# Optimization experiments

Hardware: AMD Instinct MI355X
Metric: run time of the kernel (lower is better)

## Reference

```python
import jax, jax.numpy as jnp
import numpy as np

NFEAT, NHID, NCLASS = 256, 128, 40
N_NODES, N_EDGES = 50000, 800000
BN_EPS = 1e-5


def setup_inputs() -> dict:
    key = jax.random.key(0)
    ks = jax.random.split(key, 8)
    x = jax.random.normal(ks[0], (N_NODES, NFEAT), dtype=jnp.float32)
    edge_index = jax.random.randint(ks[1], (2, N_EDGES), 0, N_NODES, dtype=jnp.int64)
    # GCNConv layer 0: nfeat -> nhid (Glorot-ish scale)
    W0 = jax.random.normal(ks[2], (NFEAT, NHID), dtype=jnp.float32) / np.sqrt(NFEAT)
    b0 = jnp.zeros((NHID,), dtype=jnp.float32)
    # BatchNorm1d(nhid)
    gamma0 = jnp.ones((NHID,), dtype=jnp.float32)
    beta0 = jnp.zeros((NHID,), dtype=jnp.float32)
    # GCNConv last: nhid -> nclass
    W1 = jax.random.normal(ks[3], (NHID, NCLASS), dtype=jnp.float32) / np.sqrt(NHID)
    b1 = jnp.zeros((NCLASS,), dtype=jnp.float32)
    return {"x": x, "edge_index": edge_index, "W0": W0, "b0": b0,
            "gamma0": gamma0, "beta0": beta0, "W1": W1, "b1": b1}


def _gcn_conv(x, src, dst, W, b, num_nodes):
    # normalize=False GCNConv: linear transform then raw sum aggregation src->dst
    h = x @ W                                   # [N, out]
    out = jax.ops.segment_sum(h[src], dst, num_segments=num_nodes)
    return out + b


def reference(x, edge_index, W0, b0, gamma0, beta0, W1, b1):
    N = x.shape[0]
    src, dst = edge_index[0], edge_index[1]
    # layer 0 conv
    h = _gcn_conv(x, src, dst, W0, b0, N)       # [N, nhid]
    # BatchNorm1d (training-mode batch stats, biased variance)
    mu = h.mean(axis=0)
    var = jnp.mean((h - mu) ** 2, axis=0)
    h = gamma0 * (h - mu) * jax.lax.rsqrt(var + BN_EPS) + beta0
    h = jax.nn.relu(h)
    # (dropout skipped: deterministic eval baseline)
    # last conv (early-return path in original forward)
    out = _gcn_conv(h, src, dst, W1, b1, N)     # [N, nclass]
    return out
```

## Files before the change

kernel.cpp:

```cpp
#include <hip/hip_runtime.h>
#include <hip/hip_fp8.h>

#define NFEAT 256
#define NHID 128
#define NCLASS 40
#define NNODES 50000
#define NEDGES 800000
#define BN_EPS 1e-5f
#define NBK 196
#define NBLK 100
#define EPB 8000
#define BKCAP 6144
#define NW1 6250
#define GEMM1_BLOCKS 1563

typedef __attribute__((ext_vector_type(4))) float f32x4;
typedef __attribute__((ext_vector_type(8))) short bf16x8;

__device__ inline ushort f2bf(float f) {
    uint u = __float_as_uint(f);
    u += 0x7FFF + ((u >> 16) & 1);
    return (ushort)(u >> 16);
}
__device__ inline float bflo(uint v) { return __uint_as_float(v << 16); }
__device__ inline float bfhi(uint v) { return __uint_as_float(v & 0xFFFF0000u); }

__device__ inline uint pk_fp8x4(float a0, float a1, float a2, float a3) {
#if __has_builtin(__builtin_amdgcn_cvt_pk_fp8_f32)
    int u = 0;
    u = __builtin_amdgcn_cvt_pk_fp8_f32(a0, a1, u, false);
    u = __builtin_amdgcn_cvt_pk_fp8_f32(a2, a3, u, true);
    return (uint)u;
#else
    __hip_fp8_e4m3 q0(a0), q1(a1), q2(a2), q3(a3);
    return (uint)q0.__x | ((uint)q1.__x << 8) | ((uint)q2.__x << 16) | ((uint)q3.__x << 24);
#endif
}
__device__ inline float fp8lo(uint v) {
#if __has_builtin(__builtin_amdgcn_cvt_f32_fp8)
    return __builtin_amdgcn_cvt_f32_fp8((int)v, 0);
#else
    __hip_fp8_e4m3 q; q.__x = (__hip_fp8_storage_t)(v & 0xFF); return (float)q;
#endif
}
__device__ inline float fp8hi(uint v) {
#if __has_builtin(__builtin_amdgcn_cvt_f32_fp8)
    return __builtin_amdgcn_cvt_f32_fp8((int)v, 1);
#else
    __hip_fp8_e4m3 q; q.__x = (__hip_fp8_storage_t)((v >> 8) & 0xFF); return (float)q;
#endif
}

__global__ void k_prep(const float* __restrict__ W0, ushort* __restrict__ W0F,
                       const int* __restrict__ ei, int* __restrict__ bcnt) {
    __shared__ int cnt[NBK];
    if (blockIdx.x < 16) {
        const int t = blockIdx.x * 256 + threadIdx.x;
        const int lane = t & 63;
        const int grp = t >> 6;
        const int kc = grp & 7, fi = grp >> 3;
        const int n = fi * 16 + (lane & 15);
        const int k0 = kc * 32 + (lane >> 4) * 8;
        ushort v[8];
        #pragma unroll
        for (int j = 0; j < 8; ++j) v[j] = f2bf(W0[(k0 + j) * NHID + n]);
        uint4 u;
        u.x = (uint)v[0] | ((uint)v[1] << 16);
        u.y = (uint)v[2] | ((uint)v[3] << 16);
        u.z = (uint)v[4] | ((uint)v[5] << 16);
        u.w = (uint)v[6] | ((uint)v[7] << 16);
        *(uint4*)&W0F[(grp * 64 + lane) * 8] = u;
    } else {
        const int blk = blockIdx.x - 16;
        const int t = threadIdx.x;
        if (t < NBK) cnt[t] = 0;
        __syncthreads();
        const int base = blk * EPB;
        for (int i = t; i < EPB; i += 256)
            atomicAdd(&cnt[ei[NEDGES + base + i] >> 8], 1);
        __syncthreads();
        if (t < NBK) bcnt[blk * NBK + t] = cnt[t];
    }
}

__global__ void k_bkscan(const int* __restrict__ bcnt, int* __restrict__ off,
                         int* __restrict__ bstart, int* __restrict__ rowptr,
                         float* __restrict__ stats) {
    __shared__ int sc[256];
    const int t = threadIdx.x;
    stats[t] = 0.f;
    int tot = 0;
    if (t < NBK)
        for (int b = 0; b < NBLK; ++b) tot += bcnt[b * NBK + t];
    sc[t] = tot;
    __syncthreads();
    for (int o = 1; o < 256; o <<= 1) {
        const int v = (t >= o) ? sc[t - o] : 0;
        __syncthreads();
        sc[t] += v;
        __syncthreads();
    }
    const int excl = sc[t] - tot;
    if (t < NBK) bstart[t] = excl;
    else if (t == NBK) bstart[NBK] = sc[NBK - 1];
    if (t == 0) rowptr[NNODES] = NEDGES;
    if (t < NBK) {
        int run = excl;
        for (int b = 0; b < NBLK; ++b) { off[b * NBK + t] = run; run += bcnt[b * NBK + t]; }
    }
}

__launch_bounds__(256, 1)
__global__ void k_scatter_gemm1(const int* __restrict__ ei, const int* __restrict__ off,
                                uint* __restrict__ packed,
                                const float* __restrict__ x, const ushort* __restrict__ W0F,
                                uchar* __restrict__ h1) {
    __shared__ int cur[NBK];
    if (blockIdx.x < NBLK) {
        const int t = threadIdx.x, blk = blockIdx.x;
        if (t < NBK) cur[t] = off[blk * NBK + t];
        __syncthreads();
        const int base = blk * EPB;
        for (int i = t; i < EPB; i += 256) {
            const int src = ei[base + i];
            const int dst = ei[NEDGES + base + i];
            const int pos = atomicAdd(&cur[dst >> 8], 1);
            packed[pos] = (uint)src | ((uint)(dst & 255) << 16);
        }
    } else {
        const int gt = (blockIdx.x - NBLK) * 256 + threadIdx.x;
        const int w = gt >> 6;
        if (w >= NW1) return;
        const int lane = gt & 63;
        const int half = w & 1;
        const int node = (w >> 1) * 16 + (lane & 15);
        const int nclamp = node < NNODES ? node : NNODES - 1;
        const float* xg = &x[(long)nclamp * NFEAT + (lane >> 4) * 8];

        float4 xa[8], xb[8];
        #pragma unroll
        for (int kc = 0; kc < 8; ++kc) {
            xa[kc] = *(const float4*)(xg + kc * 32);
            xb[kc] = *(const float4*)(xg + kc * 32 + 4);
        }
        __builtin_amdgcn_sched_barrier(0);
        bf16x8 xf[8];
        #pragma unroll
        for (int kc = 0; kc < 8; ++kc) {
            xf[kc][0]=(short)f2bf(xa[kc].x); xf[kc][1]=(short)f2bf(xa[kc].y);
            xf[kc][2]=(short)f2bf(xa[kc].z); xf[kc][3]=(short)f2bf(xa[kc].w);
            xf[kc][4]=(short)f2bf(xb[kc].x); xf[kc][5]=(short)f2bf(xb[kc].y);
            xf[kc][6]=(short)f2bf(xb[kc].z); xf[kc][7]=(short)f2bf(xb[kc].w);
        }
        __builtin_amdgcn_sched_barrier(0);
        f32x4 acc[4];
        #pragma unroll
        for (int f = 0; f < 4; ++f) acc[f] = (f32x4){0.f, 0.f, 0.f, 0.f};
        const ushort* wbase = &W0F[(size_t)lane * 8];
        #pragma unroll
        for (int kc = 0; kc < 8; ++kc) {
            #pragma unroll
            for (int f = 0; f < 4; ++f) {
                const int grp = (half * 4 + f) * 8 + kc;
                const bf16x8 wf = *(const bf16x8*)&wbase[(size_t)grp * 64 * 8];
                acc[f] = __builtin_amdgcn_mfma_f32_16x16x32_bf16(wf, xf[kc], acc[f], 0, 0, 0);
            }
        }
        if (node < NNODES) {
            const int nq = (lane >> 4) * 4;
            uchar* hp = &h1[(long)node * NHID + half * 64 + nq];
            #pragma unroll
            for (int f = 0; f < 4; ++f)
                *(uint*)&hp[f * 16] = pk_fp8x4(acc[f][0], acc[f][1], acc[f][2], acc[f][3]);
        }
    }
}

__launch_bounds__(256)
__global__ void k_bksort(const uint* __restrict__ packed, const int* __restrict__ bstart,
                         int* __restrict__ esrc, int* __restrict__ rowptr) {
    __shared__ uint pr[BKCAP];
    __shared__ int cnt[256], sc[256], cur[256];
    const int t = threadIdx.x, b = blockIdx.x;
    const int nb = bstart[b], ne = bstart[b + 1];
    const int n = ne - nb;
    cnt[t] = 0;
    __syncthreads();
    for (int i = t; i < n; i += 256) {
        const uint p = packed[nb + i];
        pr[i] = p;
        atomicAdd(&cnt[p >> 16], 1);
    }
    __syncthreads();
    const int v = cnt[t];
    sc[t] = v;
    __syncthreads();
    for (int o = 1; o < 256; o <<= 1) {
        const int tmp = (t >= o) ? sc[t - o] : 0;
        __syncthreads();
        sc[t] += tmp;
        __syncthreads();
    }
    const int excl = sc[t] - v;
    cur[t] = excl;
    const int node = (b << 8) + t;
    if (node < NNODES) rowptr[node] = nb + excl;
    __syncthreads();
    for (int i = t; i < n; i += 256) {
        const uint p = pr[i];
        const int pos = atomicAdd(&cur[p >> 16], 1);
        esrc[nb + pos] = (int)(p & 0xFFFFu);
    }
}

__launch_bounds__(256)
__global__ void k_gather1(const int* __restrict__ rowptr, const int* __restrict__ esrc,
                          const uchar* __restrict__ h1, const float* __restrict__ b0,
                          float* __restrict__ agg1) {
    const int w = (blockIdx.x * blockDim.x + threadIdx.x) >> 6;
    const int lane = threadIdx.x & 63;
    if (w >= NNODES) return;
    const int beg = rowptr[w], end = rowptr[w + 1];
    const int f = lane * 2;
    float2 acc = *(const float2*)&b0[f];
    int i = beg;
    for (; i + 7 < end; i += 8) {
        uint v[8];
        #pragma unroll
        for (int j = 0; j < 8; ++j)
            v[j] = (uint)*(const ushort*)&h1[(long)esrc[i + j] * NHID + f];
        #pragma unroll
        for (int j = 0; j < 8; ++j) { acc.x += fp8lo(v[j]); acc.y += fp8hi(v[j]); }
    }
    for (; i < end; ++i) {
        const uint v = (uint)*(const ushort*)&h1[(long)esrc[i] * NHID + f];
        acc.x += fp8lo(v); acc.y += fp8hi(v);
    }
    *(float2*)&agg1[(long)w * NHID + f] = acc;
}

__global__ void k_bnstats(const float* __restrict__ agg1,
                          float* __restrict__ sums, float* __restrict__ sumsq) {
    __shared__ float sd[256 * 4], sd2[256 * 4];
    const int t = threadIdx.x;
    const int c4 = (t & 31) * 4;
    const int rr = t >> 5;
    float4 s = make_float4(0.f,0.f,0.f,0.f), s2 = s;
    for (int r = blockIdx.x * 8 + rr; r < NNODES; r += gridDim.x * 8) {
        const float4 v = *(const float4*)&agg1[(long)r * NHID + c4];
        s.x += v.x; s.y += v.y; s.z += v.z; s.w += v.w;
        s2.x += v.x*v.x; s2.y += v.y*v.y; s2.z += v.z*v.z; s2.w += v.w*v.w;
    }
    *(float4*)&sd[t * 4] = s; *(float4*)&sd2[t * 4] = s2;
    __syncthreads();
    if (t < 32) {
        #pragma unroll
        for (int j = 1; j < 8; ++j) {
            const float4 a = *(const float4*)&sd[(j * 32 + t) * 4];
            const float4 a2 = *(const float4*)&sd2[(j * 32 + t) * 4];
            s = *(float4*)&sd[t * 4];
            s2 = *(float4*)&sd2[t * 4];
            s.x += a.x; s.y += a.y; s.z += a.z; s.w += a.w;
            s2.x += a2.x; s2.y += a2.y; s2.z += a2.z; s2.w += a2.w;
            *(float4*)&sd[t * 4] = s; *(float4*)&sd2[t * 4] = s2;
        }
        atomicAdd(&sums[c4 + 0], s.x);  atomicAdd(&sums[c4 + 1], s.y);
        atomicAdd(&sums[c4 + 2], s.z);  atomicAdd(&sums[c4 + 3], s.w);
        atomicAdd(&sumsq[c4 + 0], s2.x); atomicAdd(&sumsq[c4 + 1], s2.y);
        atomicAdd(&sumsq[c4 + 2], s2.z); atomicAdd(&sumsq[c4 + 3], s2.w);
    }
}

__launch_bounds__(256)
__global__ void k_gemm2(const float* __restrict__ agg1, const float* __restrict__ W1,
                        const float* __restrict__ sums, const float* __restrict__ sumsq,
                        const float* __restrict__ gamma, const float* __restrict__ beta,
                        ushort* __restrict__ h2) {
    __shared__ float xs[64 * 132];
    __shared__ float wt[40 * 132];
    __shared__ float s_scale[128], s_shift[128];
    const int t = threadIdx.x;
    const int base = blockIdx.x * 64;

    if (t < NHID) {
        const float mu = sums[t] * (1.f / NNODES);
        float var = sumsq[t] * (1.f / NNODES) - mu * mu;
        var = fmaxf(var, 0.f);
        const float sc = gamma[t] * rsqrtf(var + BN_EPS);
        s_scale[t] = sc;
        s_shift[t] = beta[t] - mu * sc;
    }
    for (int idx = t; idx < NHID * NCLASS; idx += 256) {
        const int c = idx / NCLASS, j = idx % NCLASS;
        wt[j * 132 + c] = W1[idx];
    }
    __syncthreads();
    {
        const int cc = (t & 31) * 4;
        const float4 sc = *(const float4*)&s_scale[cc];
        const float4 sh = *(const float4*)&s_shift[cc];
        const int rb = t >> 5;
        #pragma unroll
        for (int p = 0; p < 8; ++p) {
            const int row = p * 8 + rb;
            const int g = base + row;
            float4 v = make_float4(0.f, 0.f, 0.f, 0.f);
            if (g < NNODES) {
                const float4 a = *(const float4*)&agg1[(long)g * NHID + cc];
                v.x = fmaxf(a.x * sc.x + sh.x, 0.f);
                v.y = fmaxf(a.y * sc.y + sh.y, 0.f);
                v.z = fmaxf(a.z * sc.z + sh.z, 0.f);
                v.w = fmaxf(a.w * sc.w + sh.w, 0.f);
            }
            *(float4*)&xs[row * 132 + cc] = v;
        }
    }
    __syncthreads();

    const int node = t >> 2;
    const int j0 = (t & 3) * 10;
    float acc[10] = {};
    for (int c4 = 0; c4 < 32; ++c4) {
        const int c = c4 * 4;
        const float4 a = *(const float4*)&xs[node * 132 + c];
        #pragma unroll
        for (int jj = 0; jj < 10; ++jj) {
            const float4 wv = *(const float4*)&wt[(j0 + jj) * 132 + c];
            acc[jj] += a.x * wv.x + a.y * wv.y + a.z * wv.z + a.w * wv.w;
        }
    }
    const int g = base + node;
    if (g < NNODES) {
        #pragma unroll
        for (int p = 0; p < 5; ++p) {
            uint u = (uint)f2bf(acc[2 * p]) | ((uint)f2bf(acc[2 * p + 1]) << 16);
            *(uint*)&h2[(long)g * NCLASS + j0 + 2 * p] = u;
        }
    }
}

__launch_bounds__(256)
__global__ void k_gather2(const int* __restrict__ rowptr, const int* __restrict__ esrc,
                          const ushort* __restrict__ h2, const float* __restrict__ b1,
                          float* __restrict__ out) {
    const int t = threadIdx.x;
    if (t >= 240) return;
    const int node = blockIdx.x * 12 + t / 20;
    if (node >= NNODES) return;
    const int f = (t % 20) * 2;
    const int beg = rowptr[node], end = rowptr[node + 1];
    float2 acc = make_float2(b1[f], b1[f + 1]);
    int i = beg;
    for (; i + 3 < end; i += 4) {
        const uint v0 = *(const uint*)&h2[(long)esrc[i]     * NCLASS + f];
        const uint v1 = *(const uint*)&h2[(long)esrc[i + 1] * NCLASS + f];
        const uint v2 = *(const uint*)&h2[(long)esrc[i + 2] * NCLASS + f];
        const uint v3 = *(const uint*)&h2[(long)esrc[i + 3] * NCLASS + f];
        acc.x += (bflo(v0) + bflo(v1)) + (bflo(v2) + bflo(v3));
        acc.y += (bfhi(v0) + bfhi(v1)) + (bfhi(v2) + bfhi(v3));
    }
    for (; i < end; ++i) {
        const uint v = *(const uint*)&h2[(long)esrc[i] * NCLASS + f];
        acc.x += bflo(v); acc.y += bfhi(v);
    }
    *(float2*)&out[(long)node * NCLASS + f] = acc;
}

extern "C" void kernel_launch(void* const* d_in, const int* in_sizes, int n_in,
                              void* d_out, int out_size, void* d_ws, size_t ws_size,
                              hipStream_t stream) {
    const float* x      = (const float*)d_in[0];
    const int*   ei     = (const int*)d_in[1];
    const float* W0     = (const float*)d_in[2];
    const float* b0     = (const float*)d_in[3];
    const float* gamma0 = (const float*)d_in[4];
    const float* beta0  = (const float*)d_in[5];
    const float* W1     = (const float*)d_in[6];
    const float* b1     = (const float*)d_in[7];
    float* out = (float*)d_out;

    char* ws = (char*)d_ws;
    float* sums  = (float*)ws;
    float* sumsq = sums + 128;
    int* wsI     = (int*)(ws + 4096);
    int* rowptr  = wsI;
    int* esrc    = wsI + 50048;
    int* bcnt    = wsI + 850048;
    int* off     = wsI + 869696;
    int* bstart  = wsI + 889344;
    ushort* W0F  = (ushort*)(ws + 3563520);
    uchar* h1    = (uchar*)(ws + 3629056);
    float* agg1  = (float*)(ws + 16429056);
    uint* packed = (uint*)agg1;
    ushort* h2   = (ushort*)h1;

    k_prep<<<16 + NBLK, 256, 0, stream>>>(W0, W0F, ei, bcnt);
    k_bkscan<<<1, 256, 0, stream>>>(bcnt, off, bstart, rowptr, sums);
    k_scatter_gemm1<<<NBLK + GEMM1_BLOCKS, 256, 0, stream>>>(ei, off, packed, x, W0F, h1);
    k_bksort<<<NBK, 256, 0, stream>>>(packed, bstart, esrc, rowptr);
    k_gather1<<<(NNODES * 64 + 255) / 256, 256, 0, stream>>>(rowptr, esrc, h1, b0, agg1);
    k_bnstats<<<256, 256, 0, stream>>>(agg1, sums, sumsq);
    k_gemm2<<<(NNODES + 63) / 64, 256, 0, stream>>>(agg1, W1, sums, sumsq, gamma0, beta0, h2);
    k_gather2<<<(NNODES + 11) / 12, 256, 0, stream>>>(rowptr, esrc, h2, b1, out);
}
```

Measured before the change: 169.2 us.

## Pre-convert x to bf16 in prep kernel and stage GEMM1 tiles through swizzled LDS

Adds an fp32-to-bf16 conversion pass for x to the k_prep kernel, writing a bf16 copy of x into workspace. The GEMM1 blocks now load 64 rows of bf16 x into LDS with an XOR swizzle, using global_load_lds when the builtin is available. Each wave then computes all 128 output features for its 16 rows instead of half of them, so x is read once per row rather than twice. The aim is to take the in-kernel conversion off the GEMM path and remove the duplicated x loads. The cost is an extra round trip of the bf16 copy through memory (one write, one read), so total traffic may not shrink.

```diff
diff --git a/kernel.cpp b/kernel.cpp
--- a/kernel.cpp
+++ b/kernel.cpp
@@ -11,8 +11,8 @@
 #define NBLK 100
 #define EPB 8000
 #define BKCAP 6144
-#define NW1 6250
-#define GEMM1_BLOCKS 1563
+#define XCVT_BLOCKS 1563
+#define GEMM1_BLOCKS 782
 
 typedef __attribute__((ext_vector_type(4))) float f32x4;
 typedef __attribute__((ext_vector_type(8))) short bf16x8;
@@ -52,7 +52,8 @@
 }
 
 __global__ void k_prep(const float* __restrict__ W0, ushort* __restrict__ W0F,
-                       const int* __restrict__ ei, int* __restrict__ bcnt) {
+                       const int* __restrict__ ei, int* __restrict__ bcnt,
+                       const float* __restrict__ x, ushort* __restrict__ xbf) {
     __shared__ int cnt[NBK];
     if (blockIdx.x < 16) {
         const int t = blockIdx.x * 256 + threadIdx.x;
@@ -70,7 +71,7 @@
         u.z = (uint)v[4] | ((uint)v[5] << 16);
         u.w = (uint)v[6] | ((uint)v[7] << 16);
         *(uint4*)&W0F[(grp * 64 + lane) * 8] = u;
-    } else {
+    } else if (blockIdx.x < 16 + NBLK) {
         const int blk = blockIdx.x - 16;
         const int t = threadIdx.x;
         if (t < NBK) cnt[t] = 0;
@@ -80,6 +81,18 @@
             atomicAdd(&cnt[ei[NEDGES + base + i] >> 8], 1);
         __syncthreads();
         if (t < NBK) bcnt[blk * NBK + t] = cnt[t];
+    } else {
+        const float4* x4 = (const float4*)x;
+        const int tid = (blockIdx.x - 16 - NBLK) * 256 + threadIdx.x;
+        for (int i = tid; i < NNODES * NFEAT / 8; i += XCVT_BLOCKS * 256) {
+            const float4 a = x4[2 * i], b = x4[2 * i + 1];
+            uint4 u;
+            u.x = (uint)f2bf(a.x) | ((uint)f2bf(a.y) << 16);
+            u.y = (uint)f2bf(a.z) | ((uint)f2bf(a.w) << 16);
+            u.z = (uint)f2bf(b.x) | ((uint)f2bf(b.y) << 16);
+            u.w = (uint)f2bf(b.z) | ((uint)f2bf(b.w) << 16);
+            *(uint4*)&xbf[(size_t)i * 8] = u;
+        }
     }
 }
 
@@ -113,10 +126,11 @@
 __launch_bounds__(256, 1)
 __global__ void k_scatter_gemm1(const int* __restrict__ ei, const int* __restrict__ off,
                                 uint* __restrict__ packed,
-                                const float* __restrict__ x, const ushort* __restrict__ W0F,
+                                const ushort* __restrict__ xbf, const ushort* __restrict__ W0F,
                                 uchar* __restrict__ h1) {
-    __shared__ int cur[NBK];
+    __shared__ __align__(16) uchar lds[32768];
     if (blockIdx.x < NBLK) {
+        int* cur = (int*)lds;
         const int t = threadIdx.x, blk = blockIdx.x;
         if (t < NBK) cur[t] = off[blk * NBK + t];
         __syncthreads();
@@ -128,50 +142,54 @@
             packed[pos] = (uint)src | ((uint)(dst & 255) << 16);
         }
     } else {
-        const int gt = (blockIdx.x - NBLK) * 256 + threadIdx.x;
-        const int w = gt >> 6;
-        if (w >= NW1) return;
-        const int lane = gt & 63;
-        const int half = w & 1;
-        const int node = (w >> 1) * 16 + (lane & 15);
-        const int nclamp = node < NNODES ? node : NNODES - 1;
-        const float* xg = &x[(long)nclamp * NFEAT + (lane >> 4) * 8];
-
-        float4 xa[8], xb[8];
+        const int t = threadIdx.x;
+        const int lane = t & 63;
+        const int wave = t >> 6;
+        const int block_row = (blockIdx.x - NBLK) * 64;
+
+        #pragma unroll
+        for (int i = 0; i < 8; ++i) {
+            const int ig = wave * 8 + i;
+            const int B = (ig * 64 + lane) * 16;
+            const int row = B >> 9;
+            const int chunk = (B >> 4) & 31;
+            const int srow = min(block_row + row, NNODES - 1);
+            const ushort* gsrc = &xbf[(size_t)srow * NFEAT + (size_t)((chunk ^ (row & 7)) * 8)];
+#if __has_builtin(__builtin_amdgcn_global_load_lds)
+            __builtin_amdgcn_global_load_lds(
+                (const __attribute__((address_space(1))) void*)gsrc,
+                (__attribute__((address_space(3))) void*)(lds + ig * 1024), 16, 0, 0);
+#else
+            *(uint4*)(lds + ig * 1024 + lane * 16) = *(const uint4*)gsrc;
+#endif
+        }
+        __syncthreads();
+
+        const int r = wave * 16 + (lane & 15);
+        const int cbase = lane >> 4;
+        f32x4 acc[8];
+        #pragma unroll
+        for (int f = 0; f < 8; ++f) acc[f] = (f32x4){0.f, 0.f, 0.f, 0.f};
+        const ushort* wbase = &W0F[(size_t)lane * 8];
+
         #pragma unroll
         for (int kc = 0; kc < 8; ++kc) {
-            xa[kc] = *(const float4*)(xg + kc * 32);
-            xb[kc] = *(const float4*)(xg + kc * 32 + 4);
-        }
-        __builtin_amdgcn_sched_barrier(0);
-        bf16x8 xf[8];
-        #pragma unroll
-        for (int kc = 0; kc < 8; ++kc) {
-            xf[kc][0]=(short)f2bf(xa[kc].x); xf[kc][1]=(short)f2bf(xa[kc].y);
-            xf[kc][2]=(short)f2bf(xa[kc].z); xf[kc][3]=(short)f2bf(xa[kc].w);
-            xf[kc][4]=(short)f2bf(xb[kc].x); xf[kc][5]=(short)f2bf(xb[kc].y);
-            xf[kc][6]=(short)f2bf(xb[kc].z); xf[kc][7]=(short)f2bf(xb[kc].w);
-        }
-        __builtin_amdgcn_sched_barrier(0);
-        f32x4 acc[4];
-        #pragma unroll
-        for (int f = 0; f < 4; ++f) acc[f] = (f32x4){0.f, 0.f, 0.f, 0.f};
-        const ushort* wbase = &W0F[(size_t)lane * 8];
-        #pragma unroll
-        for (int kc = 0; kc < 8; ++kc) {
+            const int chunk = (kc * 4 + cbase) ^ (r & 7);
+            const bf16x8 xf = *(const bf16x8*)(lds + r * 512 + chunk * 16);
             #pragma unroll
-            for (int f = 0; f < 4; ++f) {
-                const int grp = (half * 4 + f) * 8 + kc;
-                const bf16x8 wf = *(const bf16x8*)&wbase[(size_t)grp * 64 * 8];
-                acc[f] = __builtin_amdgcn_mfma_f32_16x16x32_bf16(wf, xf[kc], acc[f], 0, 0, 0);
+            for (int fi = 0; fi < 8; ++fi) {
+                const bf16x8 wf = *(const bf16x8*)&wbase[(size_t)(fi * 8 + kc) * 64 * 8];
+                acc[fi] = __builtin_amdgcn_mfma_f32_16x16x32_bf16(wf, xf, acc[fi], 0, 0, 0);
             }
         }
+
+        const int node = block_row + r;
         if (node < NNODES) {
             const int nq = (lane >> 4) * 4;
-            uchar* hp = &h1[(long)node * NHID + half * 64 + nq];
+            uchar* hp = &h1[(long)node * NHID + nq];
             #pragma unroll
-            for (int f = 0; f < 4; ++f)
-                *(uint*)&hp[f * 16] = pk_fp8x4(acc[f][0], acc[f][1], acc[f][2], acc[f][3]);
+            for (int fi = 0; fi < 8; ++fi)
+                *(uint*)&hp[fi * 16] = pk_fp8x4(acc[fi][0], acc[fi][1], acc[fi][2], acc[fi][3]);
         }
     }
 }
@@ -392,11 +410,12 @@
     uchar* h1    = (uchar*)(ws + 3629056);
     float* agg1  = (float*)(ws + 16429056);
     uint* packed = (uint*)agg1;
+    ushort* xbf  = (ushort*)(ws + 20623360);
     ushort* h2   = (ushort*)h1;
 
-    k_prep<<<16 + NBLK, 256, 0, stream>>>(W0, W0F, ei, bcnt);
+    k_prep<<<16 + NBLK + XCVT_BLOCKS, 256, 0, stream>>>(W0, W0F, ei, bcnt, x, xbf);
     k_bkscan<<<1, 256, 0, stream>>>(bcnt, off, bstart, rowptr, sums);
-    k_scatter_gemm1<<<NBLK + GEMM1_BLOCKS, 256, 0, stream>>>(ei, off, packed, x, W0F, h1);
+    k_scatter_gemm1<<<NBLK + GEMM1_BLOCKS, 256, 0, stream>>>(ei, off, packed, xbf, W0F, h1);
     k_bksort<<<NBK, 256, 0, stream>>>(packed, bstart, esrc, rowptr);
     k_gather1<<<(NNODES * 64 + 255) / 256, 256, 0, stream>>>(rowptr, esrc, h1, b0, agg1);
     k_bnstats<<<256, 256, 0, stream>>>(agg1, sums, sumsq);
```

New measurement: 174.0 us. 2.9% more time.

## Merge prep, scan, scatter, bucket sort and GEMM1 into one persistent kernel

Applied to the files above, without the earlier changes.

Four launches (W0 repack plus edge counting, bucket scan, scatter plus GEMM1, bucket sort) become one kernel. Block roles are split by block index and ordered with global atomic flags and spin-waits, and a memset clears the flags and stats. The aim is to cut launch gaps and let GEMM1 overlap the edge sort. The cost is that the spin-waits rely on the producer blocks being scheduled before the consumers, so deadlock is possible if they are not, and the bucket sort now reads packed from global memory twice and recomputes the scan in every block.

```diff
diff --git a/kernel.cpp b/kernel.cpp
--- a/kernel.cpp
+++ b/kernel.cpp
@@ -10,7 +10,6 @@
 #define NBK 196
 #define NBLK 100
 #define EPB 8000
-#define BKCAP 6144
 #define NW1 6250
 #define GEMM1_BLOCKS 1563
 
@@ -51,13 +50,29 @@
 #endif
 }
 
-__global__ void k_prep(const float* __restrict__ W0, ushort* __restrict__ W0F,
-                       const int* __restrict__ ei, int* __restrict__ bcnt) {
-    __shared__ int cnt[NBK];
-    if (blockIdx.x < 16) {
-        const int t = blockIdx.x * 256 + threadIdx.x;
-        const int lane = t & 63;
-        const int grp = t >> 6;
+__device__ inline void spin_eq(int* f, int target) {
+    while (__hip_atomic_load(f, __ATOMIC_ACQUIRE, __HIP_MEMORY_SCOPE_AGENT) != target)
+        __builtin_amdgcn_s_sleep(8);
+}
+__device__ inline void release_inc(int* f) {
+    __hip_atomic_fetch_add(f, 1, __ATOMIC_RELEASE, __HIP_MEMORY_SCOPE_AGENT);
+}
+
+__launch_bounds__(256)
+__global__ void k_mega(const float* __restrict__ W0, ushort* __restrict__ W0F,
+                       const int* __restrict__ ei, int* __restrict__ bcnt,
+                       uint* __restrict__ packed, int* __restrict__ esrc,
+                       int* __restrict__ rowptr,
+                       const float* __restrict__ x, uchar* __restrict__ h1,
+                       int* __restrict__ flags) {
+    __shared__ int s_cnt[256], s_sc[256], s_cur[256];
+    __shared__ int s_seg[2];
+    int* f0 = flags; int* f1 = flags + 1; int* f2 = flags + 2;
+    const int bid = blockIdx.x, tid = threadIdx.x;
+
+    if (bid < 16) {
+        const int t = bid * 256 + tid;
+        const int lane = t & 63, grp = t >> 6;
         const int kc = grp & 7, fi = grp >> 3;
         const int n = fi * 16 + (lane & 15);
         const int k0 = kc * 32 + (lane >> 4) * 8;
@@ -70,146 +85,147 @@
         u.z = (uint)v[4] | ((uint)v[5] << 16);
         u.w = (uint)v[6] | ((uint)v[7] << 16);
         *(uint4*)&W0F[(grp * 64 + lane) * 8] = u;
-    } else {
-        const int blk = blockIdx.x - 16;
-        const int t = threadIdx.x;
-        if (t < NBK) cnt[t] = 0;
-        __syncthreads();
+        if (bid == 0 && tid == 0) rowptr[NNODES] = NEDGES;
+        __threadfence();
+        __syncthreads();
+        if (tid == 0) release_inc(f0);
+        return;
+    }
+
+    if (bid < 16 + NBLK) {
+        const int blk = bid - 16;
         const int base = blk * EPB;
-        for (int i = t; i < EPB; i += 256)
-            atomicAdd(&cnt[ei[NEDGES + base + i] >> 8], 1);
-        __syncthreads();
-        if (t < NBK) bcnt[blk * NBK + t] = cnt[t];
-    }
-}
-
-__global__ void k_bkscan(const int* __restrict__ bcnt, int* __restrict__ off,
-                         int* __restrict__ bstart, int* __restrict__ rowptr,
-                         float* __restrict__ stats) {
-    __shared__ int sc[256];
-    const int t = threadIdx.x;
-    stats[t] = 0.f;
-    int tot = 0;
-    if (t < NBK)
-        for (int b = 0; b < NBLK; ++b) tot += bcnt[b * NBK + t];
-    sc[t] = tot;
-    __syncthreads();
-    for (int o = 1; o < 256; o <<= 1) {
-        const int v = (t >= o) ? sc[t - o] : 0;
-        __syncthreads();
-        sc[t] += v;
-        __syncthreads();
-    }
-    const int excl = sc[t] - tot;
-    if (t < NBK) bstart[t] = excl;
-    else if (t == NBK) bstart[NBK] = sc[NBK - 1];
-    if (t == 0) rowptr[NNODES] = NEDGES;
-    if (t < NBK) {
-        int run = excl;
-        for (int b = 0; b < NBLK; ++b) { off[b * NBK + t] = run; run += bcnt[b * NBK + t]; }
-    }
-}
-
-__launch_bounds__(256, 1)
-__global__ void k_scatter_gemm1(const int* __restrict__ ei, const int* __restrict__ off,
-                                uint* __restrict__ packed,
-                                const float* __restrict__ x, const ushort* __restrict__ W0F,
-                                uchar* __restrict__ h1) {
-    __shared__ int cur[NBK];
-    if (blockIdx.x < NBLK) {
-        const int t = threadIdx.x, blk = blockIdx.x;
-        if (t < NBK) cur[t] = off[blk * NBK + t];
-        __syncthreads();
-        const int base = blk * EPB;
-        for (int i = t; i < EPB; i += 256) {
+        if (tid < NBK) s_cnt[tid] = 0;
+        __syncthreads();
+        for (int i = tid; i < EPB; i += 256)
+            atomicAdd(&s_cnt[ei[NEDGES + base + i] >> 8], 1);
+        __syncthreads();
+        if (tid < NBK) bcnt[blk * NBK + tid] = s_cnt[tid];
+        __threadfence();
+        __syncthreads();
+        if (tid == 0) { release_inc(f1); spin_eq(f1, NBLK); }
+        __syncthreads();
+        int tot = 0, pre = 0;
+        if (tid < NBK) {
+            for (int bb = 0; bb < NBLK; ++bb) {
+                const int v = bcnt[bb * NBK + tid];
+                tot += v;
+                if (bb < blk) pre += v;
+            }
+        }
+        s_sc[tid] = tot;
+        __syncthreads();
+        for (int o = 1; o < 256; o <<= 1) {
+            const int v = (tid >= o) ? s_sc[tid - o] : 0;
+            __syncthreads();
+            s_sc[tid] += v;
+            __syncthreads();
+        }
+        s_cur[tid] = (s_sc[tid] - tot) + pre;
+        __syncthreads();
+        for (int i = tid; i < EPB; i += 256) {
             const int src = ei[base + i];
             const int dst = ei[NEDGES + base + i];
-            const int pos = atomicAdd(&cur[dst >> 8], 1);
+            const int pos = atomicAdd(&s_cur[dst >> 8], 1);
             packed[pos] = (uint)src | ((uint)(dst & 255) << 16);
         }
-    } else {
-        const int gt = (blockIdx.x - NBLK) * 256 + threadIdx.x;
-        const int w = gt >> 6;
-        if (w >= NW1) return;
-        const int lane = gt & 63;
-        const int half = w & 1;
-        const int node = (w >> 1) * 16 + (lane & 15);
-        const int nclamp = node < NNODES ? node : NNODES - 1;
-        const float* xg = &x[(long)nclamp * NFEAT + (lane >> 4) * 8];
-
-        float4 xa[8], xb[8];
-        #pragma unroll
-        for (int kc = 0; kc < 8; ++kc) {
-            xa[kc] = *(const float4*)(xg + kc * 32);
-            xb[kc] = *(const float4*)(xg + kc * 32 + 4);
-        }
-        __builtin_amdgcn_sched_barrier(0);
-        bf16x8 xf[8];
-        #pragma unroll
-        for (int kc = 0; kc < 8; ++kc) {
-            xf[kc][0]=(short)f2bf(xa[kc].x); xf[kc][1]=(short)f2bf(xa[kc].y);
-            xf[kc][2]=(short)f2bf(xa[kc].z); xf[kc][3]=(short)f2bf(xa[kc].w);
-            xf[kc][4]=(short)f2bf(xb[kc].x); xf[kc][5]=(short)f2bf(xb[kc].y);
-            xf[kc][6]=(short)f2bf(xb[kc].z); xf[kc][7]=(short)f2bf(xb[kc].w);
-        }
-        __builtin_amdgcn_sched_barrier(0);
-        f32x4 acc[4];
-        #pragma unroll
-        for (int f = 0; f < 4; ++f) acc[f] = (f32x4){0.f, 0.f, 0.f, 0.f};
-        const ushort* wbase = &W0F[(size_t)lane * 8];
-        #pragma unroll
-        for (int kc = 0; kc < 8; ++kc) {
-            #pragma unroll
-            for (int f = 0; f < 4; ++f) {
-                const int grp = (half * 4 + f) * 8 + kc;
-                const bf16x8 wf = *(const bf16x8*)&wbase[(size_t)grp * 64 * 8];
-                acc[f] = __builtin_amdgcn_mfma_f32_16x16x32_bf16(wf, xf[kc], acc[f], 0, 0, 0);
-            }
-        }
-        if (node < NNODES) {
-            const int nq = (lane >> 4) * 4;
-            uchar* hp = &h1[(long)node * NHID + half * 64 + nq];
-            #pragma unroll
-            for (int f = 0; f < 4; ++f)
-                *(uint*)&hp[f * 16] = pk_fp8x4(acc[f][0], acc[f][1], acc[f][2], acc[f][3]);
-        }
-    }
-}
-
-__launch_bounds__(256)
-__global__ void k_bksort(const uint* __restrict__ packed, const int* __restrict__ bstart,
-                         int* __restrict__ esrc, int* __restrict__ rowptr) {
-    __shared__ uint pr[BKCAP];
-    __shared__ int cnt[256], sc[256], cur[256];
-    const int t = threadIdx.x, b = blockIdx.x;
-    const int nb = bstart[b], ne = bstart[b + 1];
-    const int n = ne - nb;
-    cnt[t] = 0;
+        __threadfence();
+        __syncthreads();
+        if (tid == 0) release_inc(f2);
+        return;
+    }
+
+    if (bid < 16 + NBLK + NBK) {
+        const int b = bid - 16 - NBLK;
+        if (tid == 0) spin_eq(f2, NBLK);
+        __syncthreads();
+        int tot = 0;
+        if (tid < NBK)
+            for (int bb = 0; bb < NBLK; ++bb) tot += bcnt[bb * NBK + tid];
+        s_sc[tid] = tot;
+        __syncthreads();
+        for (int o = 1; o < 256; o <<= 1) {
+            const int v = (tid >= o) ? s_sc[tid - o] : 0;
+            __syncthreads();
+            s_sc[tid] += v;
+            __syncthreads();
+        }
+        if (tid == b) { s_seg[0] = s_sc[b] - tot; s_seg[1] = s_sc[b]; }
+        __syncthreads();
+        const int nb = s_seg[0], ne = s_seg[1], n = ne - nb;
+        s_cnt[tid] = 0;
+        __syncthreads();
+        for (int i = tid; i < n; i += 256)
+            atomicAdd(&s_cnt[packed[nb + i] >> 16], 1);
+        __syncthreads();
+        const int v = s_cnt[tid];
+        s_sc[tid] = v;
+        __syncthreads();
+        for (int o = 1; o < 256; o <<= 1) {
+            const int tmp = (tid >= o) ? s_sc[tid - o] : 0;
+            __syncthreads();
+            s_sc[tid] += tmp;
+            __syncthreads();
+        }
+        const int excl = s_sc[tid] - v;
+        s_cur[tid] = excl;
+        const int node = (b << 8) + tid;
+        if (node < NNODES) rowptr[node] = nb + excl;
+        __syncthreads();
+        for (int i = tid; i < n; i += 256) {
+            const uint p = packed[nb + i];
+            const int pos = atomicAdd(&s_cur[p >> 16], 1);
+            esrc[nb + pos] = (int)(p & 0xFFFFu);
+        }
+        return;
+    }
+
+    if (tid == 0) spin_eq(f0, 16);
     __syncthreads();
-    for (int i = t; i < n; i += 256) {
-        const uint p = packed[nb + i];
-        pr[i] = p;
-        atomicAdd(&cnt[p >> 16], 1);
-    }
-    __syncthreads();
-    const int v = cnt[t];
-    sc[t] = v;
-    __syncthreads();
-    for (int o = 1; o < 256; o <<= 1) {
-        const int tmp = (t >= o) ? sc[t - o] : 0;
-        __syncthreads();
-        sc[t] += tmp;
-        __syncthreads();
-    }
-    const int excl = sc[t] - v;
-    cur[t] = excl;
-    const int node = (b << 8) + t;
-    if (node < NNODES) rowptr[node] = nb + excl;
-    __syncthreads();
-    for (int i = t; i < n; i += 256) {
-        const uint p = pr[i];
-        const int pos = atomicAdd(&cur[p >> 16], 1);
-        esrc[nb + pos] = (int)(p & 0xFFFFu);
+    const int gt = (bid - 16 - NBLK - NBK) * 256 + tid;
+    const int w = gt >> 6;
+    if (w >= NW1) return;
+    const int lane = gt & 63;
+    const int half = w & 1;
+    const int node = (w >> 1) * 16 + (lane & 15);
+    const int nclamp = node < NNODES ? node : NNODES - 1;
+    const float* xg = &x[(long)nclamp * NFEAT + (lane >> 4) * 8];
+
+    float4 xa[8], xb[8];
+    #pragma unroll
+    for (int kc = 0; kc < 8; ++kc) {
+        xa[kc] = *(const float4*)(xg + kc * 32);
+        xb[kc] = *(const float4*)(xg + kc * 32 + 4);
+    }
+    __builtin_amdgcn_sched_barrier(0);
+    bf16x8 xf[8];
+    #pragma unroll
+    for (int kc = 0; kc < 8; ++kc) {
+        xf[kc][0]=(short)f2bf(xa[kc].x); xf[kc][1]=(short)f2bf(xa[kc].y);
+        xf[kc][2]=(short)f2bf(xa[kc].z); xf[kc][3]=(short)f2bf(xa[kc].w);
+        xf[kc][4]=(short)f2bf(xb[kc].x); xf[kc][5]=(short)f2bf(xb[kc].y);
+        xf[kc][6]=(short)f2bf(xb[kc].z); xf[kc][7]=(short)f2bf(xb[kc].w);
+    }
+    __builtin_amdgcn_sched_barrier(0);
+    f32x4 acc[4];
+    #pragma unroll
+    for (int f = 0; f < 4; ++f) acc[f] = (f32x4){0.f, 0.f, 0.f, 0.f};
+    const ushort* wbase = &W0F[(size_t)lane * 8];
+    #pragma unroll
+    for (int kc = 0; kc < 8; ++kc) {
+        #pragma unroll
+        for (int f = 0; f < 4; ++f) {
+            const int grp = (half * 4 + f) * 8 + kc;
+            const bf16x8 wf = *(const bf16x8*)&wbase[(size_t)grp * 64 * 8];
+            acc[f] = __builtin_amdgcn_mfma_f32_16x16x32_bf16(wf, xf[kc], acc[f], 0, 0, 0);
+        }
+    }
+    if (node < NNODES) {
+        const int nq = (lane >> 4) * 4;
+        uchar* hp = &h1[(long)node * NHID + half * 64 + nq];
+        #pragma unroll
+        for (int f = 0; f < 4; ++f)
+            *(uint*)&hp[f * 16] = pk_fp8x4(acc[f][0], acc[f][1], acc[f][2], acc[f][3]);
     }
 }
 
@@ -381,23 +397,23 @@
 
     char* ws = (char*)d_ws;
     float* sums  = (float*)ws;
-    float* sumsq = sums + 128;
+    float* sumsq = (float*)(ws + 512);
+    int* flags   = (int*)(ws + 1024);
     int* wsI     = (int*)(ws + 4096);
     int* rowptr  = wsI;
     int* esrc    = wsI + 50048;
     int* bcnt    = wsI + 850048;
-    int* off     = wsI + 869696;
-    int* bstart  = wsI + 889344;
+    int* bstart  = wsI + 869696;
     ushort* W0F  = (ushort*)(ws + 3563520);
     uchar* h1    = (uchar*)(ws + 3629056);
     float* agg1  = (float*)(ws + 16429056);
     uint* packed = (uint*)agg1;
     ushort* h2   = (ushort*)h1;
-
-    k_prep<<<16 + NBLK, 256, 0, stream>>>(W0, W0F, ei, bcnt);
-    k_bkscan<<<1, 256, 0, stream>>>(bcnt, off, bstart, rowptr, sums);
-    k_scatter_gemm1<<<NBLK + GEMM1_BLOCKS, 256, 0, stream>>>(ei, off, packed, x, W0F, h1);
-    k_bksort<<<NBK, 256, 0, stream>>>(packed, bstart, esrc, rowptr);
+    (void)bstart;
+
+    hipMemsetAsync(ws, 0, 1280, stream);
+    k_mega<<<16 + NBLK + NBK + GEMM1_BLOCKS, 256, 0, stream>>>(
+        W0, W0F, ei, bcnt, packed, esrc, rowptr, x, h1, flags);
     k_gather1<<<(NNODES * 64 + 255) / 256, 256, 0, stream>>>(rowptr, esrc, h1, b0, agg1);
     k_bnstats<<<256, 256, 0, stream>>>(agg1, sums, sumsq);
     k_gemm2<<<(NNODES + 63) / 64, 256, 0, stream>>>(agg1, W1, sums, sumsq, gamma0, beta0, h2);
```

After: 382.6 us. 2.26x slower.
